# Kernel optimization log

Measured on AMD Instinct MI355X. Metric: run time of the kernel, lower is better.

Reference implementation:

```python
import jax, jax.numpy as jnp
import numpy as np

B, S, E, H = 4, 2048, 1024, 8
D = E // H  # head_dim = 128


def setup_inputs() -> dict:
    key = jax.random.key(0)
    ks = jax.random.split(key, 7)
    scale = 1.0 / np.sqrt(D)
    return {
        "sequences": jax.random.normal(ks[0], (B, S, E), dtype=jnp.float32),
        # per-head Linear weights, torch layout [out, in] stacked over heads
        "Wq": jax.random.normal(ks[1], (H, D, D), dtype=jnp.float32) * scale,
        "Wk": jax.random.normal(ks[2], (H, D, D), dtype=jnp.float32) * scale,
        "Wv": jax.random.normal(ks[3], (H, D, D), dtype=jnp.float32) * scale,
        "bq": jax.random.normal(ks[4], (H, D), dtype=jnp.float32) * scale,
        "bk": jax.random.normal(ks[5], (H, D), dtype=jnp.float32) * scale,
        "bv": jax.random.normal(ks[6], (H, D), dtype=jnp.float32) * scale,
    }


def reference(sequences, Wq, Wk, Wv, bq, bk, bv):
    # split feature dim into heads: [B,S,H,D]
    xh = sequences.reshape(B, S, H, D)
    # torch Linear: y = x @ W.T + b  ->  contract input dim d with W[h, o, d]
    q = jnp.einsum("bshd,hod->bsho", xh, Wq) + bq
    k = jnp.einsum("bshd,hod->bsho", xh, Wk) + bk
    v = jnp.einsum("bshd,hod->bsho", xh, Wv) + bv
    # NOTE: original scales by 1/sqrt(num_heads), not 1/sqrt(head_dim)
    scores = jnp.einsum("bshd,bthd->bhst", q, k) / jnp.sqrt(jnp.float32(H))
    attn = jax.nn.softmax(scores, axis=-1)  # [B,H,S,S]
    out = jnp.einsum("bhst,bthd->bshd", attn, v)
    # hstack over heads == reshape back to [B,S,E]
    return out.reshape(B, S, E)
```

## Files before the change

### kernel.cpp

```cpp
#include <hip/hip_runtime.h>
#include <hip/hip_bf16.h>

#define B_ 4
#define S_ 2048
#define E_ 1024
#define H_ 8
#define D_ 128

using f16x8 = __attribute__((ext_vector_type(8))) _Float16;
using f32x4 = __attribute__((ext_vector_type(4))) float;

__device__ __forceinline__ ushort f2h_bits(float f) {
    union { _Float16 h; ushort u; } cv; cv.h = (_Float16)f; return cv.u;
}
__device__ __forceinline__ float h2f(ushort u) {
    union { ushort u; _Float16 h; } cv; cv.u = u; return (float)cv.h;
}
__device__ __forceinline__ f16x8 pack8(const float* __restrict__ p) {
    float4 f0 = *(const float4*)p;
    float4 f1 = *(const float4*)(p + 4);
    f16x8 r;
    r[0] = (_Float16)f0.x; r[1] = (_Float16)f0.y;
    r[2] = (_Float16)f0.z; r[3] = (_Float16)f0.w;
    r[4] = (_Float16)f1.x; r[5] = (_Float16)f1.y;
    r[6] = (_Float16)f1.z; r[7] = (_Float16)f1.w;
    return r;
}

__global__ __launch_bounds__(256) void kv_proj(
    const float* __restrict__ seq,
    const float* __restrict__ Wk, const float* __restrict__ Wv,
    const float* __restrict__ bk, const float* __restrict__ bv,
    ushort* __restrict__ ko, ushort* __restrict__ vo)
{
    constexpr int TS = 136;
    __shared__ ushort Tk[128 * TS];
    __shared__ ushort Tv[128 * TS];
    const int m0 = blockIdx.x * 128, h = blockIdx.y;
    const int tid = threadIdx.x, lane = tid & 63, w = tid >> 6;
    const int l16 = lane & 15, quad = lane >> 4;

    f16x8 a[2][4];
    #pragma unroll
    for (int mt = 0; mt < 2; ++mt)
        #pragma unroll
        for (int ks = 0; ks < 4; ++ks)
            a[mt][ks] = pack8(&seq[(size_t)(m0 + w * 32 + mt * 16 + l16) * E_
                                   + h * D_ + ks * 32 + quad * 8]);

    {
        const float* W = Wk + (size_t)h * D_ * D_;
        f32x4 acc[2][8];
        #pragma unroll
        for (int mt = 0; mt < 2; ++mt)
            #pragma unroll
            for (int nt = 0; nt < 8; ++nt) { f32x4 z = {0.f,0.f,0.f,0.f}; acc[mt][nt] = z; }
        #pragma unroll
        for (int ks = 0; ks < 4; ++ks)
            #pragma unroll
            for (int nt = 0; nt < 8; ++nt) {
                f16x8 bfr = pack8(&W[(size_t)(nt * 16 + l16) * D_ + ks * 32 + quad * 8]);
                #pragma unroll
                for (int mt = 0; mt < 2; ++mt)
                    acc[mt][nt] = __builtin_amdgcn_mfma_f32_16x16x32_f16(
                        a[mt][ks], bfr, acc[mt][nt], 0, 0, 0);
            }
        #pragma unroll
        for (int nt = 0; nt < 8; ++nt) {
            int o = nt * 16 + l16;
            float bias = bk[h * D_ + o];
            #pragma unroll
            for (int mt = 0; mt < 2; ++mt)
                #pragma unroll
                for (int r = 0; r < 4; ++r) {
                    int row = w * 32 + mt * 16 + quad * 4 + r;
                    Tk[row * TS + (o ^ (quad << 3))] = f2h_bits(acc[mt][nt][r] + bias);
                }
        }
    }
    {
        const float* W = Wv + (size_t)h * D_ * D_;
        f32x4 acc[2][8];
        #pragma unroll
        for (int mt = 0; mt < 2; ++mt)
            #pragma unroll
            for (int nt = 0; nt < 8; ++nt) { f32x4 z = {0.f,0.f,0.f,0.f}; acc[mt][nt] = z; }
        #pragma unroll
        for (int ks = 0; ks < 4; ++ks)
            #pragma unroll
            for (int nt = 0; nt < 8; ++nt) {
                f16x8 bfr = pack8(&W[(size_t)(nt * 16 + l16) * D_ + ks * 32 + quad * 8]);
                #pragma unroll
                for (int mt = 0; mt < 2; ++mt)
                    acc[mt][nt] = __builtin_amdgcn_mfma_f32_16x16x32_f16(
                        a[mt][ks], bfr, acc[mt][nt], 0, 0, 0);
            }
        #pragma unroll
        for (int nt = 0; nt < 8; ++nt) {
            int o = nt * 16 + l16;
            float bias = bv[h * D_ + o];
            #pragma unroll
            for (int mt = 0; mt < 2; ++mt)
                #pragma unroll
                for (int r = 0; r < 4; ++r) {
                    int row = w * 32 + mt * 16 + quad * 4 + r;
                    Tv[o * TS + row] = f2h_bits(acc[mt][nt][r] + bias);
                }
        }
    }
    __syncthreads();

    #pragma unroll
    for (int i = 0; i < 8; ++i) {
        int idx = tid + i * 256;
        int row = idx >> 4, c8 = (idx & 15) * 8;
        uint4 dk = *(uint4*)&Tk[row * TS + (c8 ^ (((row >> 2) & 3) << 3))];
        int m = m0 + row, bi = m >> 11, s = m & (S_ - 1);
        *(uint4*)&ko[(((size_t)bi * H_ + h) * S_ + s) * D_ + c8] = dk;
        uint4 dv = *(uint4*)&Tv[row * TS + c8];
        int mg = m0 + c8, bv_i = mg >> 11, s0 = mg & (S_ - 1);
        *(uint4*)&vo[(((size_t)bv_i * H_ + h) * D_ + row) * S_ + s0] = dv;
    }
}

__global__ __launch_bounds__(256) void attn(
    const float* __restrict__ seq, const float* __restrict__ Wq,
    const float* __restrict__ bq,
    const ushort* __restrict__ kg, const ushort* __restrict__ vtg,
    float* __restrict__ out)
{
    constexpr int KS = 136;
    constexpr int VS = 136;
    __shared__ alignas(16) ushort smem[128 * KS + 128 * VS];
    ushort* const Klds = smem;
    ushort* const Vt   = smem + 128 * KS;

    const int m0 = blockIdx.x * 128;
    const int h = blockIdx.y, bi = blockIdx.z;
    const int bh = bi * H_ + h;
    const int tid = threadIdx.x, lane = tid & 63, w = tid >> 6;
    const int l16 = lane & 15, quad = lane >> 4;
    const size_t baseK = (size_t)bh * S_ * D_;
    const size_t baseV = (size_t)bh * D_ * S_;
    const float qscale = 0.35355339059327373f * 1.4426950408889634f;
    const int qq_r = (l16 >> 2) & 3;

    {
        f16x8 xa[2][4];
        #pragma unroll
        for (int mt = 0; mt < 2; ++mt)
            #pragma unroll
            for (int ks = 0; ks < 4; ++ks)
                xa[mt][ks] = pack8(&seq[((size_t)bi * S_ + m0 + w * 32 + mt * 16 + l16) * E_
                                        + h * D_ + ks * 32 + quad * 8]);
        f32x4 qacc[2][8];
        #pragma unroll
        for (int mt = 0; mt < 2; ++mt)
            #pragma unroll
            for (int nt = 0; nt < 8; ++nt) { f32x4 z = {0.f,0.f,0.f,0.f}; qacc[mt][nt] = z; }
        const float* W = Wq + (size_t)h * D_ * D_;
        #pragma unroll
        for (int ks = 0; ks < 4; ++ks)
            #pragma unroll
            for (int nt = 0; nt < 8; ++nt) {
                f16x8 bfr = pack8(&W[(size_t)(nt * 16 + l16) * D_ + ks * 32 + quad * 8]);
                #pragma unroll
                for (int mt = 0; mt < 2; ++mt)
                    qacc[mt][nt] = __builtin_amdgcn_mfma_f32_16x16x32_f16(
                        xa[mt][ks], bfr, qacc[mt][nt], 0, 0, 0);
            }
        #pragma unroll
        for (int nt = 0; nt < 8; ++nt) {
            int o = nt * 16 + l16;
            float bias = bq[h * D_ + o];
            #pragma unroll
            for (int mt = 0; mt < 2; ++mt)
                #pragma unroll
                for (int r = 0; r < 4; ++r) {
                    int row = w * 32 + mt * 16 + quad * 4 + r;
                    Klds[row * KS + (o ^ (quad << 3))] =
                        f2h_bits((qacc[mt][nt][r] + bias) * qscale);
                }
        }
    }
    __syncthreads();

    f16x8 qf[2][4];
    #pragma unroll
    for (int mt = 0; mt < 2; ++mt)
        #pragma unroll
        for (int ks = 0; ks < 4; ++ks)
            qf[mt][ks] = *(const f16x8*)&Klds[(w * 32 + mt * 16 + l16) * KS
                                              + ks * 32 + ((quad ^ qq_r) << 3)];

    f32x4 o_acc[2][8];
    #pragma unroll
    for (int mt = 0; mt < 2; ++mt)
        #pragma unroll
        for (int nt = 0; nt < 8; ++nt) { f32x4 z = {0.f,0.f,0.f,0.f}; o_acc[mt][nt] = z; }
    float m_prev[2][4], l_lane[2][4];
    #pragma unroll
    for (int mt = 0; mt < 2; ++mt)
        #pragma unroll
        for (int r = 0; r < 4; ++r) { m_prev[mt][r] = -1e30f; l_lane[mt][r] = 0.f; }

    for (int j = 0; j < S_ / 128; ++j) {
        const int n0 = j * 128;
        __syncthreads();
        #pragma unroll
        for (int i = 0; i < 8; ++i) {
            int idx = tid + i * 256;
            int r = idx >> 4, c8 = (idx & 15) * 8;
            *(uint4*)&Klds[r * KS + c8] =
                *(const uint4*)&kg[baseK + (size_t)(n0 + r) * D_ + c8];
        }
        #pragma unroll
        for (int i = 0; i < 8; ++i) {
            int idx = tid + i * 256;
            int d = idx >> 4, c8 = (idx & 15) * 8;
            *(uint4*)&Vt[d * VS + c8] =
                *(const uint4*)&vtg[baseV + (size_t)d * S_ + n0 + c8];
        }
        __syncthreads();

        f32x4 sacc[2][8];
        #pragma unroll
        for (int mt = 0; mt < 2; ++mt)
            #pragma unroll
            for (int nt = 0; nt < 8; ++nt) { f32x4 z = {0.f,0.f,0.f,0.f}; sacc[mt][nt] = z; }
        #pragma unroll
        for (int ks = 0; ks < 4; ++ks)
            #pragma unroll
            for (int nt = 0; nt < 8; ++nt) {
                f16x8 kf = *(const f16x8*)&Klds[(nt * 16 + l16) * KS + ks * 32 + quad * 8];
                #pragma unroll
                for (int mt = 0; mt < 2; ++mt)
                    sacc[mt][nt] = __builtin_amdgcn_mfma_f32_16x16x32_f16(
                        qf[mt][ks], kf, sacc[mt][nt], 0, 0, 0);
            }

        #pragma unroll
        for (int mt = 0; mt < 2; ++mt)
            #pragma unroll
            for (int r = 0; r < 4; ++r) {
                float mx = sacc[mt][0][r];
                #pragma unroll
                for (int nt = 1; nt < 8; ++nt) mx = fmaxf(mx, sacc[mt][nt][r]);
                #pragma unroll
                for (int d = 1; d < 16; d <<= 1)
                    mx = fmaxf(mx, __shfl_xor(mx, d));
                float mnew  = fmaxf(m_prev[mt][r], mx);
                float alpha = exp2f(m_prev[mt][r] - mnew);
                m_prev[mt][r] = mnew;
                float sumr = 0.f;
                #pragma unroll
                for (int nt = 0; nt < 8; ++nt) {
                    ushort u = f2h_bits(exp2f(sacc[mt][nt][r] - mnew));
                    sumr += h2f(u);
                    sacc[mt][nt][r] = __uint_as_float((unsigned)u);
                }
                l_lane[mt][r] = l_lane[mt][r] * alpha + sumr;
                #pragma unroll
                for (int nt = 0; nt < 8; ++nt)
                    o_acc[mt][nt][r] *= alpha;
            }

        __syncthreads();
        #pragma unroll
        for (int mt = 0; mt < 2; ++mt)
            #pragma unroll
            for (int r = 0; r < 4; ++r) {
                int row = w * 32 + mt * 16 + quad * 4 + r;
                #pragma unroll
                for (int nt = 0; nt < 8; ++nt) {
                    int col = nt * 16 + l16;
                    Klds[row * KS + (col ^ (quad << 3))] =
                        (ushort)__float_as_uint(sacc[mt][nt][r]);
                }
            }

        #pragma unroll
        for (int ks = 0; ks < 4; ++ks) {
            f16x8 pa[2];
            #pragma unroll
            for (int mt = 0; mt < 2; ++mt)
                pa[mt] = *(const f16x8*)&Klds[(w * 32 + mt * 16 + l16) * KS
                                              + ks * 32 + ((quad ^ qq_r) << 3)];
            #pragma unroll
            for (int nt = 0; nt < 8; ++nt) {
                f16x8 vf = *(const f16x8*)&Vt[(nt * 16 + l16) * VS + ks * 32 + quad * 8];
                #pragma unroll
                for (int mt = 0; mt < 2; ++mt)
                    o_acc[mt][nt] = __builtin_amdgcn_mfma_f32_16x16x32_f16(
                        pa[mt], vf, o_acc[mt][nt], 0, 0, 0);
            }
        }
    }

    #pragma unroll
    for (int mt = 0; mt < 2; ++mt)
        #pragma unroll
        for (int r = 0; r < 4; ++r) {
            float l = l_lane[mt][r];
            #pragma unroll
            for (int d = 1; d < 16; d <<= 1)
                l += __shfl_xor(l, d);
            float rinv = 1.0f / l;
            int srow = m0 + w * 32 + mt * 16 + quad * 4 + r;
            #pragma unroll
            for (int nt = 0; nt < 8; ++nt) {
                int col = nt * 16 + l16;
                out[((size_t)bi * S_ + srow) * E_ + h * D_ + col] =
                    o_acc[mt][nt][r] * rinv;
            }
        }
}

extern "C" void kernel_launch(void* const* d_in, const int* in_sizes, int n_in,
                              void* d_out, int out_size, void* d_ws, size_t ws_size,
                              hipStream_t stream) {
    const float* seq = (const float*)d_in[0];
    const float* Wq  = (const float*)d_in[1];
    const float* Wk  = (const float*)d_in[2];
    const float* Wv  = (const float*)d_in[3];
    const float* bq  = (const float*)d_in[4];
    const float* bk  = (const float*)d_in[5];
    const float* bv  = (const float*)d_in[6];

    const size_t per = (size_t)B_ * H_ * S_ * D_;
    if (ws_size < 2 * per * sizeof(ushort)) return;
    ushort* kws  = (ushort*)d_ws;
    ushort* vtws = kws + per;

    kv_proj<<<dim3(B_ * S_ / 128, H_), 256, 0, stream>>>(
        seq, Wk, Wv, bk, bv, kws, vtws);
    attn<<<dim3(S_ / 128, H_, B_), 256, 0, stream>>>(
        seq, Wq, bq, kws, vtws, (float*)d_out);
}
```

Baseline: 309.6 us.

## Read K/V fragments straight from global memory and drop LDS staging and barriers

The attention kernel no longer stages K and V tiles in shared memory each iteration. It loads MFMA fragments directly from global/L2, which removes the per-iteration __syncthreads and shrinks LDS to a single per-wave P buffer. The grid is flattened so heads of the same query tile are adjacent, launch bounds request 2 waves/occupancy, and kv_proj uses 64-row tiles with one reused LDS buffer for higher occupancy. The softmax row sum now uses the fp32 probabilities instead of fp16-rounded ones. In exchange, each wave issues redundant uncoalesced global loads of K/V (4x the traffic of shared staging), relying on cache hits.

```diff
diff --git a/kernel.cpp b/kernel.cpp
--- a/kernel.cpp
+++ b/kernel.cpp
@@ -12,9 +12,6 @@
 
 __device__ __forceinline__ ushort f2h_bits(float f) {
     union { _Float16 h; ushort u; } cv; cv.h = (_Float16)f; return cv.u;
-}
-__device__ __forceinline__ float h2f(ushort u) {
-    union { ushort u; _Float16 h; } cv; cv.u = u; return (float)cv.h;
 }
 __device__ __forceinline__ f16x8 pack8(const float* __restrict__ p) {
     float4 f0 = *(const float4*)p;
@@ -27,116 +24,101 @@
     return r;
 }
 
-__global__ __launch_bounds__(256) void kv_proj(
+__global__ __launch_bounds__(256, 4) void kv_proj(
     const float* __restrict__ seq,
     const float* __restrict__ Wk, const float* __restrict__ Wv,
     const float* __restrict__ bk, const float* __restrict__ bv,
     ushort* __restrict__ ko, ushort* __restrict__ vo)
 {
-    constexpr int TS = 136;
-    __shared__ ushort Tk[128 * TS];
-    __shared__ ushort Tv[128 * TS];
-    const int m0 = blockIdx.x * 128, h = blockIdx.y;
+    __shared__ alignas(16) ushort T[128 * 72];
+    const int m0 = blockIdx.x * 64, h = blockIdx.y;
     const int tid = threadIdx.x, lane = tid & 63, w = tid >> 6;
     const int l16 = lane & 15, quad = lane >> 4;
-
-    f16x8 a[2][4];
-    #pragma unroll
-    for (int mt = 0; mt < 2; ++mt)
-        #pragma unroll
-        for (int ks = 0; ks < 4; ++ks)
-            a[mt][ks] = pack8(&seq[(size_t)(m0 + w * 32 + mt * 16 + l16) * E_
-                                   + h * D_ + ks * 32 + quad * 8]);
+    const int bi = m0 >> 11, sbase = m0 & (S_ - 1);
+
+    f16x8 a[4];
+    #pragma unroll
+    for (int ks = 0; ks < 4; ++ks)
+        a[ks] = pack8(&seq[(size_t)(m0 + w * 16 + l16) * E_ + h * D_ + ks * 32 + quad * 8]);
 
     {
         const float* W = Wk + (size_t)h * D_ * D_;
-        f32x4 acc[2][8];
-        #pragma unroll
-        for (int mt = 0; mt < 2; ++mt)
-            #pragma unroll
-            for (int nt = 0; nt < 8; ++nt) { f32x4 z = {0.f,0.f,0.f,0.f}; acc[mt][nt] = z; }
+        f32x4 acc[8];
+        #pragma unroll
+        for (int nt = 0; nt < 8; ++nt) { f32x4 z = {0.f,0.f,0.f,0.f}; acc[nt] = z; }
         #pragma unroll
         for (int ks = 0; ks < 4; ++ks)
             #pragma unroll
             for (int nt = 0; nt < 8; ++nt) {
                 f16x8 bfr = pack8(&W[(size_t)(nt * 16 + l16) * D_ + ks * 32 + quad * 8]);
-                #pragma unroll
-                for (int mt = 0; mt < 2; ++mt)
-                    acc[mt][nt] = __builtin_amdgcn_mfma_f32_16x16x32_f16(
-                        a[mt][ks], bfr, acc[mt][nt], 0, 0, 0);
+                acc[nt] = __builtin_amdgcn_mfma_f32_16x16x32_f16(a[ks], bfr, acc[nt], 0, 0, 0);
             }
         #pragma unroll
         for (int nt = 0; nt < 8; ++nt) {
             int o = nt * 16 + l16;
             float bias = bk[h * D_ + o];
             #pragma unroll
-            for (int mt = 0; mt < 2; ++mt)
-                #pragma unroll
-                for (int r = 0; r < 4; ++r) {
-                    int row = w * 32 + mt * 16 + quad * 4 + r;
-                    Tk[row * TS + (o ^ (quad << 3))] = f2h_bits(acc[mt][nt][r] + bias);
-                }
-        }
-    }
+            for (int r = 0; r < 4; ++r) {
+                int row = w * 16 + quad * 4 + r;
+                T[row * 136 + (o ^ (quad << 3))] = f2h_bits(acc[nt][r] + bias);
+            }
+        }
+    }
+    __syncthreads();
+    #pragma unroll
+    for (int i = 0; i < 4; ++i) {
+        int idx = tid + i * 256;
+        int row = idx >> 4, c8 = (idx & 15) * 8;
+        uint4 dk = *(uint4*)&T[row * 136 + (c8 ^ (((row >> 2) & 3) << 3))];
+        *(uint4*)&ko[(((size_t)bi * H_ + h) * S_ + sbase + row) * D_ + c8] = dk;
+    }
+    __syncthreads();
     {
         const float* W = Wv + (size_t)h * D_ * D_;
-        f32x4 acc[2][8];
-        #pragma unroll
-        for (int mt = 0; mt < 2; ++mt)
-            #pragma unroll
-            for (int nt = 0; nt < 8; ++nt) { f32x4 z = {0.f,0.f,0.f,0.f}; acc[mt][nt] = z; }
+        f32x4 acc[8];
+        #pragma unroll
+        for (int nt = 0; nt < 8; ++nt) { f32x4 z = {0.f,0.f,0.f,0.f}; acc[nt] = z; }
         #pragma unroll
         for (int ks = 0; ks < 4; ++ks)
             #pragma unroll
             for (int nt = 0; nt < 8; ++nt) {
                 f16x8 bfr = pack8(&W[(size_t)(nt * 16 + l16) * D_ + ks * 32 + quad * 8]);
-                #pragma unroll
-                for (int mt = 0; mt < 2; ++mt)
-                    acc[mt][nt] = __builtin_amdgcn_mfma_f32_16x16x32_f16(
-                        a[mt][ks], bfr, acc[mt][nt], 0, 0, 0);
+                acc[nt] = __builtin_amdgcn_mfma_f32_16x16x32_f16(a[ks], bfr, acc[nt], 0, 0, 0);
             }
         #pragma unroll
         for (int nt = 0; nt < 8; ++nt) {
             int o = nt * 16 + l16;
             float bias = bv[h * D_ + o];
             #pragma unroll
-            for (int mt = 0; mt < 2; ++mt)
-                #pragma unroll
-                for (int r = 0; r < 4; ++r) {
-                    int row = w * 32 + mt * 16 + quad * 4 + r;
-                    Tv[o * TS + row] = f2h_bits(acc[mt][nt][r] + bias);
-                }
+            for (int r = 0; r < 4; ++r) {
+                int row = w * 16 + quad * 4 + r;
+                T[o * 72 + row] = f2h_bits(acc[nt][r] + bias);
+            }
         }
     }
     __syncthreads();
-
-    #pragma unroll
-    for (int i = 0; i < 8; ++i) {
+    #pragma unroll
+    for (int i = 0; i < 4; ++i) {
         int idx = tid + i * 256;
-        int row = idx >> 4, c8 = (idx & 15) * 8;
-        uint4 dk = *(uint4*)&Tk[row * TS + (c8 ^ (((row >> 2) & 3) << 3))];
-        int m = m0 + row, bi = m >> 11, s = m & (S_ - 1);
-        *(uint4*)&ko[(((size_t)bi * H_ + h) * S_ + s) * D_ + c8] = dk;
-        uint4 dv = *(uint4*)&Tv[row * TS + c8];
-        int mg = m0 + c8, bv_i = mg >> 11, s0 = mg & (S_ - 1);
-        *(uint4*)&vo[(((size_t)bv_i * H_ + h) * D_ + row) * S_ + s0] = dv;
-    }
-}
-
-__global__ __launch_bounds__(256) void attn(
+        int d = idx >> 3, c8 = (idx & 7) * 8;
+        uint4 dv = *(uint4*)&T[d * 72 + c8];
+        *(uint4*)&vo[(((size_t)bi * H_ + h) * D_ + d) * S_ + sbase + c8] = dv;
+    }
+}
+
+__global__ __launch_bounds__(256, 2) void attn(
     const float* __restrict__ seq, const float* __restrict__ Wq,
     const float* __restrict__ bq,
     const ushort* __restrict__ kg, const ushort* __restrict__ vtg,
     float* __restrict__ out)
 {
-    constexpr int KS = 136;
-    constexpr int VS = 136;
-    __shared__ alignas(16) ushort smem[128 * KS + 128 * VS];
-    ushort* const Klds = smem;
-    ushort* const Vt   = smem + 128 * KS;
-
-    const int m0 = blockIdx.x * 128;
-    const int h = blockIdx.y, bi = blockIdx.z;
+    constexpr int PS = 136;
+    __shared__ alignas(16) ushort Plds[128 * PS];
+
+    const int bid = blockIdx.x;
+    const int h  = bid & 7;
+    const int m0 = ((bid >> 3) & 15) * 128;
+    const int bi = bid >> 7;
     const int bh = bi * H_ + h;
     const int tid = threadIdx.x, lane = tid & 63, w = tid >> 6;
     const int l16 = lane & 15, quad = lane >> 4;
@@ -178,19 +160,17 @@
                 #pragma unroll
                 for (int r = 0; r < 4; ++r) {
                     int row = w * 32 + mt * 16 + quad * 4 + r;
-                    Klds[row * KS + (o ^ (quad << 3))] =
+                    Plds[row * PS + (o ^ (quad << 3))] =
                         f2h_bits((qacc[mt][nt][r] + bias) * qscale);
                 }
         }
     }
-    __syncthreads();
-
     f16x8 qf[2][4];
     #pragma unroll
     for (int mt = 0; mt < 2; ++mt)
         #pragma unroll
         for (int ks = 0; ks < 4; ++ks)
-            qf[mt][ks] = *(const f16x8*)&Klds[(w * 32 + mt * 16 + l16) * KS
+            qf[mt][ks] = *(const f16x8*)&Plds[(w * 32 + mt * 16 + l16) * PS
                                               + ks * 32 + ((quad ^ qq_r) << 3)];
 
     f32x4 o_acc[2][8];
@@ -206,22 +186,6 @@
 
     for (int j = 0; j < S_ / 128; ++j) {
         const int n0 = j * 128;
-        __syncthreads();
-        #pragma unroll
-        for (int i = 0; i < 8; ++i) {
-            int idx = tid + i * 256;
-            int r = idx >> 4, c8 = (idx & 15) * 8;
-            *(uint4*)&Klds[r * KS + c8] =
-                *(const uint4*)&kg[baseK + (size_t)(n0 + r) * D_ + c8];
-        }
-        #pragma unroll
-        for (int i = 0; i < 8; ++i) {
-            int idx = tid + i * 256;
-            int d = idx >> 4, c8 = (idx & 15) * 8;
-            *(uint4*)&Vt[d * VS + c8] =
-                *(const uint4*)&vtg[baseV + (size_t)d * S_ + n0 + c8];
-        }
-        __syncthreads();
 
         f32x4 sacc[2][8];
         #pragma unroll
@@ -232,7 +196,8 @@
         for (int ks = 0; ks < 4; ++ks)
             #pragma unroll
             for (int nt = 0; nt < 8; ++nt) {
-                f16x8 kf = *(const f16x8*)&Klds[(nt * 16 + l16) * KS + ks * 32 + quad * 8];
+                f16x8 kf = *(const f16x8*)&kg[baseK + (size_t)(n0 + nt * 16 + l16) * D_
+                                              + ks * 32 + quad * 8];
                 #pragma unroll
                 for (int mt = 0; mt < 2; ++mt)
                     sacc[mt][nt] = __builtin_amdgcn_mfma_f32_16x16x32_f16(
@@ -255,9 +220,9 @@
                 float sumr = 0.f;
                 #pragma unroll
                 for (int nt = 0; nt < 8; ++nt) {
-                    ushort u = f2h_bits(exp2f(sacc[mt][nt][r] - mnew));
-                    sumr += h2f(u);
-                    sacc[mt][nt][r] = __uint_as_float((unsigned)u);
+                    float p = exp2f(sacc[mt][nt][r] - mnew);
+                    sumr += p;
+                    sacc[mt][nt][r] = __uint_as_float((unsigned)f2h_bits(p));
                 }
                 l_lane[mt][r] = l_lane[mt][r] * alpha + sumr;
                 #pragma unroll
@@ -265,7 +230,6 @@
                     o_acc[mt][nt][r] *= alpha;
             }
 
-        __syncthreads();
         #pragma unroll
         for (int mt = 0; mt < 2; ++mt)
             #pragma unroll
@@ -274,7 +238,7 @@
                 #pragma unroll
                 for (int nt = 0; nt < 8; ++nt) {
                     int col = nt * 16 + l16;
-                    Klds[row * KS + (col ^ (quad << 3))] =
+                    Plds[row * PS + (col ^ (quad << 3))] =
                         (ushort)__float_as_uint(sacc[mt][nt][r]);
                 }
             }
@@ -284,11 +248,12 @@
             f16x8 pa[2];
             #pragma unroll
             for (int mt = 0; mt < 2; ++mt)
-                pa[mt] = *(const f16x8*)&Klds[(w * 32 + mt * 16 + l16) * KS
+                pa[mt] = *(const f16x8*)&Plds[(w * 32 + mt * 16 + l16) * PS
                                               + ks * 32 + ((quad ^ qq_r) << 3)];
             #pragma unroll
             for (int nt = 0; nt < 8; ++nt) {
-                f16x8 vf = *(const f16x8*)&Vt[(nt * 16 + l16) * VS + ks * 32 + quad * 8];
+                f16x8 vf = *(const f16x8*)&vtg[baseV + (size_t)(nt * 16 + l16) * S_
+                                               + n0 + ks * 32 + quad * 8];
                 #pragma unroll
                 for (int mt = 0; mt < 2; ++mt)
                     o_acc[mt][nt] = __builtin_amdgcn_mfma_f32_16x16x32_f16(
@@ -332,8 +297,8 @@
     ushort* kws  = (ushort*)d_ws;
     ushort* vtws = kws + per;
 
-    kv_proj<<<dim3(B_ * S_ / 128, H_), 256, 0, stream>>>(
+    kv_proj<<<dim3(B_ * S_ / 64, H_), 256, 0, stream>>>(
         seq, Wk, Wv, bk, bv, kws, vtws);
-    attn<<<dim3(S_ / 128, H_, B_), 256, 0, stream>>>(
+    attn<<<512, 256, 0, stream>>>(
         seq, Wq, bq, kws, vtws, (float*)d_out);
 }
```

Measured after the change: 440.1 us. 42.2% more time.

## Pre-swizzle K/V images in global memory and load them with direct global-to-LDS DMA

Applied to the files above, without the earlier changes.

The projection kernel now writes K and a tiled V-transpose in an XOR-swizzled 128x128 layout, so the attention kernel can copy each tile straight into LDS with global_load_lds instead of staging it through registers. The padded LDS layout is replaced by an XOR swizzle shared by K, P and V reads. kv_proj also stages the weight matrices in LDS instead of reloading and converting them from global for every fragment. The softmax row sum now uses the fp32 probabilities rather than their fp16-rounded values, and launch bounds request two blocks per CU. The risks are correctness of the swizzle and DMA lane mapping, and register pressure under the tighter launch bound.

```diff
diff --git a/kernel.cpp b/kernel.cpp
--- a/kernel.cpp
+++ b/kernel.cpp
@@ -12,9 +12,6 @@
 
 __device__ __forceinline__ ushort f2h_bits(float f) {
     union { _Float16 h; ushort u; } cv; cv.h = (_Float16)f; return cv.u;
-}
-__device__ __forceinline__ float h2f(ushort u) {
-    union { ushort u; _Float16 h; } cv; cv.u = u; return (float)cv.h;
 }
 __device__ __forceinline__ f16x8 pack8(const float* __restrict__ p) {
     float4 f0 = *(const float4*)p;
@@ -27,29 +24,48 @@
     return r;
 }
 
-__global__ __launch_bounds__(256) void kv_proj(
+#define GLD_LDS(gp, lp)                                                      \
+    __builtin_amdgcn_global_load_lds(                                        \
+        (const __attribute__((address_space(1))) void*)(gp),                 \
+        (__attribute__((address_space(3))) void*)(lp), 16, 0, 0)
+
+
+__global__ __launch_bounds__(256, 2) void kv_proj(
     const float* __restrict__ seq,
     const float* __restrict__ Wk, const float* __restrict__ Wv,
     const float* __restrict__ bk, const float* __restrict__ bv,
     ushort* __restrict__ ko, ushort* __restrict__ vo)
 {
-    constexpr int TS = 136;
-    __shared__ ushort Tk[128 * TS];
-    __shared__ ushort Tv[128 * TS];
+    __shared__ alignas(16) ushort Ws[128 * 128];
+    __shared__ alignas(16) ushort Timg[128 * 128];
     const int m0 = blockIdx.x * 128, h = blockIdx.y;
     const int tid = threadIdx.x, lane = tid & 63, w = tid >> 6;
     const int l16 = lane & 15, quad = lane >> 4;
-
-    f16x8 a[2][4];
-    #pragma unroll
-    for (int mt = 0; mt < 2; ++mt)
-        #pragma unroll
-        for (int ks = 0; ks < 4; ++ks)
-            a[mt][ks] = pack8(&seq[(size_t)(m0 + w * 32 + mt * 16 + l16) * E_
-                                   + h * D_ + ks * 32 + quad * 8]);
+    const int bh = ((m0 >> 11) * H_) + h;
+    const int sbase = m0 & (S_ - 1);
+    const int tile = sbase >> 7;
+
+    f16x8 xa[2][4];
+    #pragma unroll
+    for (int mt = 0; mt < 2; ++mt)
+        #pragma unroll
+        for (int ks = 0; ks < 4; ++ks)
+            xa[mt][ks] = pack8(&seq[(size_t)(m0 + w * 32 + mt * 16 + l16) * E_
+                                    + h * D_ + ks * 32 + quad * 8]);
 
     {
         const float* W = Wk + (size_t)h * D_ * D_;
+        #pragma unroll
+        for (int i = 0; i < 8; ++i) {
+            int idx = tid + i * 256;
+            int o = idx >> 4, c8 = (idx & 15) * 8;
+            f16x8 d = pack8(&W[(size_t)o * D_ + c8]);
+            *(f16x8*)&Ws[o * 128 + ((((c8 >> 3) ^ (o & 7))) << 3)] = d;
+        }
+    }
+    __syncthreads();
+
+    {
         f32x4 acc[2][8];
         #pragma unroll
         for (int mt = 0; mt < 2; ++mt)
@@ -59,11 +75,12 @@
         for (int ks = 0; ks < 4; ++ks)
             #pragma unroll
             for (int nt = 0; nt < 8; ++nt) {
-                f16x8 bfr = pack8(&W[(size_t)(nt * 16 + l16) * D_ + ks * 32 + quad * 8]);
+                f16x8 bfr = *(const f16x8*)&Ws[(nt * 16 + l16) * 128
+                                               + (((ks * 4 + quad) ^ (l16 & 7)) << 3)];
                 #pragma unroll
                 for (int mt = 0; mt < 2; ++mt)
                     acc[mt][nt] = __builtin_amdgcn_mfma_f32_16x16x32_f16(
-                        a[mt][ks], bfr, acc[mt][nt], 0, 0, 0);
+                        xa[mt][ks], bfr, acc[mt][nt], 0, 0, 0);
             }
         #pragma unroll
         for (int nt = 0; nt < 8; ++nt) {
@@ -74,12 +91,33 @@
                 #pragma unroll
                 for (int r = 0; r < 4; ++r) {
                     int row = w * 32 + mt * 16 + quad * 4 + r;
-                    Tk[row * TS + (o ^ (quad << 3))] = f2h_bits(acc[mt][nt][r] + bias);
-                }
-        }
+                    Timg[row * 128 + ((((o >> 3) ^ (row & 7))) << 3) + (o & 7)] =
+                        f2h_bits(acc[mt][nt][r] + bias);
+                }
+        }
+    }
+    __syncthreads();
+
+    #pragma unroll
+    for (int i = 0; i < 8; ++i) {
+        int idx = tid + i * 256;
+        int row = idx >> 4, c8 = (idx & 15) * 8;
+        *(uint4*)&ko[((size_t)bh * S_ + sbase + row) * D_ + c8] =
+            *(uint4*)&Timg[row * 128 + c8];
     }
     {
         const float* W = Wv + (size_t)h * D_ * D_;
+        #pragma unroll
+        for (int i = 0; i < 8; ++i) {
+            int idx = tid + i * 256;
+            int o = idx >> 4, c8 = (idx & 15) * 8;
+            f16x8 d = pack8(&W[(size_t)o * D_ + c8]);
+            *(f16x8*)&Ws[o * 128 + ((((c8 >> 3) ^ (o & 7))) << 3)] = d;
+        }
+    }
+    __syncthreads();
+
+    {
         f32x4 acc[2][8];
         #pragma unroll
         for (int mt = 0; mt < 2; ++mt)
@@ -89,11 +127,12 @@
         for (int ks = 0; ks < 4; ++ks)
             #pragma unroll
             for (int nt = 0; nt < 8; ++nt) {
-                f16x8 bfr = pack8(&W[(size_t)(nt * 16 + l16) * D_ + ks * 32 + quad * 8]);
+                f16x8 bfr = *(const f16x8*)&Ws[(nt * 16 + l16) * 128
+                                               + (((ks * 4 + quad) ^ (l16 & 7)) << 3)];
                 #pragma unroll
                 for (int mt = 0; mt < 2; ++mt)
                     acc[mt][nt] = __builtin_amdgcn_mfma_f32_16x16x32_f16(
-                        a[mt][ks], bfr, acc[mt][nt], 0, 0, 0);
+                        xa[mt][ks], bfr, acc[mt][nt], 0, 0, 0);
             }
         #pragma unroll
         for (int nt = 0; nt < 8; ++nt) {
@@ -104,36 +143,29 @@
                 #pragma unroll
                 for (int r = 0; r < 4; ++r) {
                     int row = w * 32 + mt * 16 + quad * 4 + r;
-                    Tv[o * TS + row] = f2h_bits(acc[mt][nt][r] + bias);
+                    Timg[o * 128 + ((((row >> 3) ^ (o & 7))) << 3) + (row & 7)] =
+                        f2h_bits(acc[mt][nt][r] + bias);
                 }
         }
     }
     __syncthreads();
-
     #pragma unroll
     for (int i = 0; i < 8; ++i) {
         int idx = tid + i * 256;
-        int row = idx >> 4, c8 = (idx & 15) * 8;
-        uint4 dk = *(uint4*)&Tk[row * TS + (c8 ^ (((row >> 2) & 3) << 3))];
-        int m = m0 + row, bi = m >> 11, s = m & (S_ - 1);
-        *(uint4*)&ko[(((size_t)bi * H_ + h) * S_ + s) * D_ + c8] = dk;
-        uint4 dv = *(uint4*)&Tv[row * TS + c8];
-        int mg = m0 + c8, bv_i = mg >> 11, s0 = mg & (S_ - 1);
-        *(uint4*)&vo[(((size_t)bv_i * H_ + h) * D_ + row) * S_ + s0] = dv;
-    }
-}
-
-__global__ __launch_bounds__(256) void attn(
+        int d = idx >> 4, c8 = (idx & 15) * 8;
+        *(uint4*)&vo[(((size_t)bh * 16 + tile) * 128 + d) * 128 + c8] =
+            *(uint4*)&Timg[d * 128 + c8];
+    }
+}
+
+__global__ __launch_bounds__(256, 2) void attn(
     const float* __restrict__ seq, const float* __restrict__ Wq,
     const float* __restrict__ bq,
     const ushort* __restrict__ kg, const ushort* __restrict__ vtg,
     float* __restrict__ out)
 {
-    constexpr int KS = 136;
-    constexpr int VS = 136;
-    __shared__ alignas(16) ushort smem[128 * KS + 128 * VS];
-    ushort* const Klds = smem;
-    ushort* const Vt   = smem + 128 * KS;
+    __shared__ alignas(16) ushort KP[128 * 128];
+    __shared__ alignas(16) ushort Vimg[128 * 128];
 
     const int m0 = blockIdx.x * 128;
     const int h = blockIdx.y, bi = blockIdx.z;
@@ -141,9 +173,7 @@
     const int tid = threadIdx.x, lane = tid & 63, w = tid >> 6;
     const int l16 = lane & 15, quad = lane >> 4;
     const size_t baseK = (size_t)bh * S_ * D_;
-    const size_t baseV = (size_t)bh * D_ * S_;
     const float qscale = 0.35355339059327373f * 1.4426950408889634f;
-    const int qq_r = (l16 >> 2) & 3;
 
     {
         f16x8 xa[2][4];
@@ -178,20 +208,18 @@
                 #pragma unroll
                 for (int r = 0; r < 4; ++r) {
                     int row = w * 32 + mt * 16 + quad * 4 + r;
-                    Klds[row * KS + (o ^ (quad << 3))] =
+                    KP[row * 128 + ((((o >> 3) ^ (row & 7))) << 3) + (o & 7)] =
                         f2h_bits((qacc[mt][nt][r] + bias) * qscale);
                 }
         }
     }
-    __syncthreads();
-
     f16x8 qf[2][4];
     #pragma unroll
     for (int mt = 0; mt < 2; ++mt)
         #pragma unroll
         for (int ks = 0; ks < 4; ++ks)
-            qf[mt][ks] = *(const f16x8*)&Klds[(w * 32 + mt * 16 + l16) * KS
-                                              + ks * 32 + ((quad ^ qq_r) << 3)];
+            qf[mt][ks] = *(const f16x8*)&KP[(w * 32 + mt * 16 + l16) * 128
+                                            + (((ks * 4 + quad) ^ (l16 & 7)) << 3)];
 
     f32x4 o_acc[2][8];
     #pragma unroll
@@ -208,19 +236,14 @@
         const int n0 = j * 128;
         __syncthreads();
         #pragma unroll
-        for (int i = 0; i < 8; ++i) {
-            int idx = tid + i * 256;
-            int r = idx >> 4, c8 = (idx & 15) * 8;
-            *(uint4*)&Klds[r * KS + c8] =
-                *(const uint4*)&kg[baseK + (size_t)(n0 + r) * D_ + c8];
-        }
-        #pragma unroll
-        for (int i = 0; i < 8; ++i) {
-            int idx = tid + i * 256;
-            int d = idx >> 4, c8 = (idx & 15) * 8;
-            *(uint4*)&Vt[d * VS + c8] =
-                *(const uint4*)&vtg[baseV + (size_t)d * S_ + n0 + c8];
-        }
+        for (int t = 0; t < 8; ++t)
+            GLD_LDS(kg + baseK + (size_t)(n0 + w * 32 + t * 4) * 128 + lane * 8,
+                    &KP[(w * 32 + t * 4) * 128]);
+        const size_t baseV = ((size_t)bh * 16 + j) * 128 * 128;
+        #pragma unroll
+        for (int t = 0; t < 8; ++t)
+            GLD_LDS(vtg + baseV + (size_t)(w * 32 + t * 4) * 128 + lane * 8,
+                    &Vimg[(w * 32 + t * 4) * 128]);
         __syncthreads();
 
         f32x4 sacc[2][8];
@@ -232,7 +255,8 @@
         for (int ks = 0; ks < 4; ++ks)
             #pragma unroll
             for (int nt = 0; nt < 8; ++nt) {
-                f16x8 kf = *(const f16x8*)&Klds[(nt * 16 + l16) * KS + ks * 32 + quad * 8];
+                f16x8 kf = *(const f16x8*)&KP[(nt * 16 + l16) * 128
+                                              + (((ks * 4 + quad) ^ (l16 & 7)) << 3)];
                 #pragma unroll
                 for (int mt = 0; mt < 2; ++mt)
                     sacc[mt][nt] = __builtin_amdgcn_mfma_f32_16x16x32_f16(
@@ -255,9 +279,9 @@
                 float sumr = 0.f;
                 #pragma unroll
                 for (int nt = 0; nt < 8; ++nt) {
-                    ushort u = f2h_bits(exp2f(sacc[mt][nt][r] - mnew));
-                    sumr += h2f(u);
-                    sacc[mt][nt][r] = __uint_as_float((unsigned)u);
+                    float p = exp2f(sacc[mt][nt][r] - mnew);
+                    sumr += p;
+                    sacc[mt][nt][r] = __uint_as_float((unsigned)f2h_bits(p));
                 }
                 l_lane[mt][r] = l_lane[mt][r] * alpha + sumr;
                 #pragma unroll
@@ -274,7 +298,7 @@
                 #pragma unroll
                 for (int nt = 0; nt < 8; ++nt) {
                     int col = nt * 16 + l16;
-                    Klds[row * KS + (col ^ (quad << 3))] =
+                    KP[row * 128 + ((((col >> 3) ^ (row & 7))) << 3) + (col & 7)] =
                         (ushort)__float_as_uint(sacc[mt][nt][r]);
                 }
             }
@@ -284,11 +308,12 @@
             f16x8 pa[2];
             #pragma unroll
             for (int mt = 0; mt < 2; ++mt)
-                pa[mt] = *(const f16x8*)&Klds[(w * 32 + mt * 16 + l16) * KS
-                                              + ks * 32 + ((quad ^ qq_r) << 3)];
-            #pragma unroll
-            for (int nt = 0; nt < 8; ++nt) {
-                f16x8 vf = *(const f16x8*)&Vt[(nt * 16 + l16) * VS + ks * 32 + quad * 8];
+                pa[mt] = *(const f16x8*)&KP[(w * 32 + mt * 16 + l16) * 128
+                                            + (((ks * 4 + quad) ^ (l16 & 7)) << 3)];
+            #pragma unroll
+            for (int nt = 0; nt < 8; ++nt) {
+                f16x8 vf = *(const f16x8*)&Vimg[(nt * 16 + l16) * 128
+                                                + (((ks * 4 + quad) ^ (l16 & 7)) << 3)];
                 #pragma unroll
                 for (int mt = 0; mt < 2; ++mt)
                     o_acc[mt][nt] = __builtin_amdgcn_mfma_f32_16x16x32_f16(
```

After: 339.5 us. 9.7% more time.
